# Kernel optimization log

Measured on AMD Instinct MI355X. Metric: run time of the kernel, lower is better.

The kernel has to match this reference:

```python
import jax, jax.numpy as jnp
import numpy as np

D_MODEL = 1024
N_HEADS = 16
HEAD_DIM = D_MODEL // N_HEADS


def setup_inputs() -> dict:
    key = jax.random.key(0)
    ks = jax.random.split(key, 6)
    B, S = 2, 2048
    scale = 1.0 / np.sqrt(D_MODEL)
    x = jax.random.normal(ks[0], (B, S, D_MODEL), dtype=jnp.float32)
    Wq = jax.random.normal(ks[1], (D_MODEL, D_MODEL), dtype=jnp.float32) * scale
    Wk = jax.random.normal(ks[2], (D_MODEL, D_MODEL), dtype=jnp.float32) * scale
    Wv = jax.random.normal(ks[3], (D_MODEL, D_MODEL), dtype=jnp.float32) * scale
    Wo = jax.random.normal(ks[4], (D_MODEL, D_MODEL), dtype=jnp.float32) * scale
    bo = jax.random.normal(ks[5], (D_MODEL,), dtype=jnp.float32) * 0.02
    return {"x": x, "Wq": Wq, "Wk": Wk, "Wv": Wv, "Wo": Wo, "bo": bo}


def reference(x, Wq, Wk, Wv, Wo, bo):
    B, S, _ = x.shape
    H, hd = N_HEADS, HEAD_DIM
    # qkv projections (no bias, qkv_bias=False)
    q = (x @ Wq).reshape(B, S, H, hd).transpose(0, 2, 1, 3)  # [B,H,S,hd]
    k = (x @ Wk).reshape(B, S, H, hd).transpose(0, 2, 1, 3)
    v = (x @ Wv).reshape(B, S, H, hd).transpose(0, 2, 1, 3)
    scores = jnp.einsum('bhqd,bhkd->bhqk', q, k)  # [B,H,S,S]
    causal = jnp.tril(jnp.ones((S, S), dtype=bool))  # True = keep
    scores = jnp.where(causal, scores, -jnp.inf)
    weights = jax.nn.softmax(scores / np.sqrt(hd), axis=-1)
    # dropout p=0.0 -> identity
    ctx = jnp.einsum('bhqk,bhkd->bhqd', weights, v)  # [B,H,S,hd]
    ctx = ctx.transpose(0, 2, 1, 3).reshape(B, S, H * hd)
    return ctx @ Wo + bo
```

## Files before the change

### kernel.cpp

```cpp
#include <hip/hip_runtime.h>
#include <hip/hip_bf16.h>
#include <stdint.h>

#define SEQ    2048
#define BATCH  2
#define DMODEL 1024
#define NHEADS 16
#define HDIM   64
#define MROWS  (BATCH*SEQ)

typedef __attribute__((ext_vector_type(8))) short bf16x8;
typedef __attribute__((ext_vector_type(4))) short bf16x4;
typedef __attribute__((ext_vector_type(4))) float f32x4;

__device__ inline void global_to_lds16(const void* g, void* l) {
  __builtin_amdgcn_global_load_lds(
      (const __attribute__((address_space(1))) uint32_t*)g,
      (__attribute__((address_space(3))) uint32_t*)l, 16, 0, 0);
}

__device__ inline unsigned short f2bf_bits(float f) {
  __hip_bfloat16 h = __float2bfloat16(f);
  return *(unsigned short*)&h;
}

__global__ void prep_kernel(const float* __restrict__ x, __hip_bfloat16* __restrict__ xb,
                            const float* __restrict__ Wq, const float* __restrict__ Wk,
                            const float* __restrict__ Wv, const float* __restrict__ Wo,
                            __hip_bfloat16* __restrict__ Wqkv_t, __hip_bfloat16* __restrict__ Wo_t) {
  __shared__ float tile[32][33];
  if (blockIdx.x < 4096) {
    int i = (blockIdx.x * 256 + threadIdx.x) * 4;
    float4 v = *(const float4*)(x + i);
    ushort4 o;
    o.x = f2bf_bits(v.x); o.y = f2bf_bits(v.y);
    o.z = f2bf_bits(v.z); o.w = f2bf_bits(v.w);
    *(ushort4*)(xb + i) = o;
    return;
  }
  int idx = blockIdx.x - 4096;
  int z = idx >> 10;
  int rem = idx & 1023;
  const float* W = (z == 0) ? Wq : (z == 1) ? Wk : (z == 2) ? Wv : Wo;
  __hip_bfloat16* dst = (z < 3) ? (Wqkv_t + (size_t)z * 1024 * 1024) : Wo_t;
  int k0 = (rem & 31) * 32, n0 = (rem >> 5) * 32;
  int tx = threadIdx.x & 31, ty = threadIdx.x >> 5;
#pragma unroll
  for (int r = 0; r < 4; r++)
    tile[ty + r * 8][tx] = W[(size_t)(k0 + ty + r * 8) * 1024 + n0 + tx];
  __syncthreads();
#pragma unroll
  for (int r = 0; r < 4; r++)
    dst[(size_t)(n0 + ty + r * 8) * 1024 + k0 + tx] = __float2bfloat16(tile[tx][ty + r * 8]);
}

template <int TN, bool OUT_BF16, int MINW, bool FUSE_VT>
__global__ __launch_bounds__(256, MINW)
void gemm_kernel(const __hip_bfloat16* __restrict__ A, const __hip_bfloat16* __restrict__ Bt,
                 void* __restrict__ C, const float* __restrict__ bias, int ldc,
                 __hip_bfloat16* __restrict__ Vt) {
  __shared__ __hip_bfloat16 Asl[2][128 * 64];
  __shared__ __hip_bfloat16 Bsl[2][TN * 64];

  const int t = threadIdx.x;
  const int lane = t & 63;
  const int w = t >> 6;
  constexpr int MI = (TN == 128) ? 4 : 2;
  const int wrow = (TN == 128) ? (w >> 1) * 64 : w * 32;
  const int wcol = (TN == 128) ? (w & 1) * 64 : 0;
  const int m0 = blockIdx.y * 128;
  const int n0 = blockIdx.x * TN;

  f32x4 acc[MI][4];
#pragma unroll
  for (int i = 0; i < MI; i++)
#pragma unroll
    for (int j = 0; j < 4; j++) acc[i][j] = (f32x4){0.f, 0.f, 0.f, 0.f};

  const int srow = lane >> 3;
  const int sjc = (lane & 7) ^ srow;
  const int fm = lane & 15;
  const int g4 = lane >> 4;

  auto stage = [&](int k0, int bufi) {
#pragma unroll
    for (int i = 0; i < 4; i++) {
      int seg = i * 4 + w;
      int r = seg * 8 + srow;
      global_to_lds16(A + (size_t)(m0 + r) * 1024 + k0 + sjc * 8,
                      (void*)(&Asl[bufi][0] + seg * 512 + lane * 8));
    }
#pragma unroll
    for (int i = 0; i < TN / 32; i++) {
      int seg = i * 4 + w;
      int r = seg * 8 + srow;
      global_to_lds16(Bt + (size_t)(n0 + r) * 1024 + k0 + sjc * 8,
                      (void*)(&Bsl[bufi][0] + seg * 512 + lane * 8));
    }
  };

  stage(0, 0);
  for (int k0 = 0; k0 < 1024; k0 += 64) {
    const int buf = (k0 >> 6) & 1;
    __syncthreads();

    bf16x8 af[2][MI], bfr[2][4];
#pragma unroll
    for (int kb = 0; kb < 2; kb++) {
#pragma unroll
      for (int mi = 0; mi < MI; mi++) {
        int row = wrow + mi * 16 + fm;
        af[kb][mi] = *(const bf16x8*)(&Asl[buf][0] + row * 64 + (((kb * 4 + g4) ^ (row & 7)) << 3));
      }
#pragma unroll
      for (int ni = 0; ni < 4; ni++) {
        int row = wcol + ni * 16 + fm;
        bfr[kb][ni] = *(const bf16x8*)(&Bsl[buf][0] + row * 64 + (((kb * 4 + g4) ^ (row & 7)) << 3));
      }
    }

    if (k0 + 64 < 1024) stage(k0 + 64, buf ^ 1);

#pragma unroll
    for (int kb = 0; kb < 2; kb++)
#pragma unroll
      for (int mi = 0; mi < MI; mi++)
#pragma unroll
        for (int ni = 0; ni < 4; ni++)
          acc[mi][ni] = __builtin_amdgcn_mfma_f32_16x16x32_bf16(af[kb][mi], bfr[kb][ni], acc[mi][ni], 0, 0, 0);
  }

  const bool vt_block = FUSE_VT && (n0 >= 2048);
#pragma unroll
  for (int mi = 0; mi < MI; mi++) {
    int mb = m0 + wrow + mi * 16 + g4 * 4;
#pragma unroll
    for (int ni = 0; ni < 4; ni++) {
      int n = n0 + wcol + ni * 16 + fm;
      if (vt_block) {
        int nv = n - 2048;
        int bhh = (mb >> 11) * 16 + (nv >> 6);
        int d = nv & 63;
        int s = mb & 2047;
        unsigned short u[4];
#pragma unroll
        for (int r = 0; r < 4; r++) u[r] = f2bf_bits(acc[mi][ni][r]);
        *(ushort4*)(Vt + ((size_t)bhh * 64 + d) * 2048 + s) = *(const ushort4*)u;
      } else {
        float bv = OUT_BF16 ? 0.f : bias[n];
#pragma unroll
        for (int r = 0; r < 4; r++) {
          if (OUT_BF16)
            ((__hip_bfloat16*)C)[(size_t)(mb + r) * ldc + n] = __float2bfloat16(acc[mi][ni][r]);
          else
            ((float*)C)[(size_t)(mb + r) * ldc + n] = acc[mi][ni][r] + bv;
        }
      }
    }
  }
}

__global__ __launch_bounds__(512, 2)
void qkv_gemm_kernel(const __hip_bfloat16* __restrict__ A,
                     const __hip_bfloat16* __restrict__ Bt,
                     __hip_bfloat16* __restrict__ QKV,
                     __hip_bfloat16* __restrict__ Vt) {
  extern __shared__ __align__(128) char smem_raw[];
  __hip_bfloat16* Asl = (__hip_bfloat16*)smem_raw;
  __hip_bfloat16* Bsl = Asl + 4 * 8192;

  const int t = threadIdx.x;
  const int lane = t & 63;
  const int w = t >> 6;
  const int wm = w >> 2;
  const int wn = w & 3;

  const int wgid = blockIdx.y * 12 + blockIdx.x;
  const int swz = (wgid & 7) * 24 + (wgid >> 3);
  const int m0 = (swz / 12) * 256;
  const int n0 = (swz % 12) * 256;

  const int fm = lane & 15;
  const int g4 = lane >> 4;
  const int rsl = ((g4 ^ ((fm >> 1) & 3)) << 3);
  const int rr = lane >> 2;
  const int cc = (lane & 3) ^ ((lane >> 3) & 3);

  f32x4 acc[8][4];
#pragma unroll
  for (int i = 0; i < 8; i++)
#pragma unroll
    for (int j = 0; j < 4; j++) acc[i][j] = (f32x4){0.f, 0.f, 0.f, 0.f};

  auto stageA = [&](int ktt, int s) {
#pragma unroll
    for (int i = 0; i < 2; i++) {
      int seg = w * 2 + i;
      global_to_lds16(A + (size_t)(m0 + seg * 16 + rr) * 1024 + ktt * 32 + cc * 8,
                      (void*)(Asl + s * 8192 + seg * 512 + lane * 8));
    }
  };
  auto stageB = [&](int ktt, int s) {
#pragma unroll
    for (int i = 0; i < 2; i++) {
      int seg = w * 2 + i;
      global_to_lds16(Bt + (size_t)(n0 + seg * 16 + rr) * 1024 + ktt * 32 + cc * 8,
                      (void*)(Bsl + s * 8192 + seg * 512 + lane * 8));
    }
  };

  stageA(0, 0); stageB(0, 0);
  stageA(1, 1); stageB(1, 1);
  stageA(2, 2); stageB(2, 2);
  asm volatile("s_waitcnt vmcnt(8)" ::: "memory");
  __builtin_amdgcn_s_barrier();

  for (int kt = 0; kt < 32; ++kt) {
    const int s = kt & 3;
    const __hip_bfloat16* Ab = Asl + s * 8192;
    const __hip_bfloat16* Bb = Bsl + s * 8192;

    bf16x8 af[4], bf[4];
#pragma unroll
    for (int mi = 0; mi < 4; mi++) {
      int row = wm * 128 + mi * 16 + fm;
      af[mi] = *(const bf16x8*)(Ab + row * 32 + rsl);
    }
#pragma unroll
    for (int ni = 0; ni < 4; ni++) {
      int row = wn * 64 + ni * 16 + fm;
      bf[ni] = *(const bf16x8*)(Bb + row * 32 + rsl);
    }
    if (kt < 29) stageA(kt + 3, (kt + 3) & 3);
    __builtin_amdgcn_s_barrier();
    __builtin_amdgcn_s_setprio(1);
#pragma unroll
    for (int mi = 0; mi < 4; mi++)
#pragma unroll
      for (int ni = 0; ni < 4; ni++)
        acc[mi][ni] = __builtin_amdgcn_mfma_f32_16x16x32_bf16(af[mi], bf[ni], acc[mi][ni], 0, 0, 0);
    __builtin_amdgcn_s_setprio(0);
    __builtin_amdgcn_s_barrier();

#pragma unroll
    for (int mi = 0; mi < 4; mi++) {
      int row = wm * 128 + (mi + 4) * 16 + fm;
      af[mi] = *(const bf16x8*)(Ab + row * 32 + rsl);
    }
    if (kt < 29) stageB(kt + 3, (kt + 3) & 3);
    __builtin_amdgcn_s_barrier();
    __builtin_amdgcn_s_setprio(1);
#pragma unroll
    for (int mi = 0; mi < 4; mi++)
#pragma unroll
      for (int ni = 0; ni < 4; ni++)
        acc[mi + 4][ni] = __builtin_amdgcn_mfma_f32_16x16x32_bf16(af[mi], bf[ni], acc[mi + 4][ni], 0, 0, 0);
    __builtin_amdgcn_s_setprio(0);
    if (kt < 29)       asm volatile("s_waitcnt vmcnt(8)" ::: "memory");
    else if (kt == 29) asm volatile("s_waitcnt vmcnt(4)" ::: "memory");
    else if (kt == 30) asm volatile("s_waitcnt vmcnt(0)" ::: "memory");
    __builtin_amdgcn_s_barrier();
  }

  const bool vt_block = (n0 >= 2048);
#pragma unroll
  for (int mi = 0; mi < 8; mi++) {
    int mb = m0 + wm * 128 + mi * 16 + g4 * 4;
#pragma unroll
    for (int ni = 0; ni < 4; ni++) {
      int n = n0 + wn * 64 + ni * 16 + fm;
      if (vt_block) {
        int nv = n - 2048;
        int bhh = (mb >> 11) * 16 + (nv >> 6);
        int d = nv & 63;
        int ssq = mb & 2047;
        unsigned short u[4];
#pragma unroll
        for (int r = 0; r < 4; r++) u[r] = f2bf_bits(acc[mi][ni][r]);
        *(ushort4*)(Vt + ((size_t)bhh * 64 + d) * 2048 + ssq) = *(const ushort4*)u;
      } else {
#pragma unroll
        for (int r = 0; r < 4; r++)
          QKV[(size_t)(mb + r) * 3072 + n] = __float2bfloat16(acc[mi][ni][r]);
      }
    }
  }
}

__global__ __launch_bounds__(256, 2)
void attn_kernel(const __hip_bfloat16* __restrict__ QKV,
                 const __hip_bfloat16* __restrict__ Vt,
                 __hip_bfloat16* __restrict__ ctx) {
  __shared__ __hip_bfloat16 Klds[2][128 * 64];
  __shared__ __hip_bfloat16 Vlds[2][64 * 128];

  const int t = threadIdx.x;
  const int lane = t & 63;
  const int w = t >> 6;
  const int L = blockIdx.x;
  const int bh = (L & 7) + 8 * ((L >> 3) & 3);
  const int jraw = L >> 5;
  const int jb = (jraw < 8) ? jraw : 23 - jraw;
  const int qtab[2] = { jb, 31 - jb };
  const int b = bh >> 4, h = bh & 15;
  const int fm = lane & 15;
  const int g4 = lane >> 4;
  const int fk = g4 * 8;
  const size_t rowb = (size_t)b * SEQ;
  const float c = 0.18033688011112042f;

  const int krr = lane >> 3;
  const int kjc = (lane & 7) ^ krr;
  const int vrr = lane >> 4;

  bf16x8 qf[2][2];
#pragma unroll
  for (int hh = 0; hh < 2; hh++) {
    const __hip_bfloat16* qp = QKV + (rowb + qtab[hh] * 64 + w * 16 + fm) * 3072 + h * 64 + fk;
    bf16x8 r0 = *(const bf16x8*)qp;
    bf16x8 r1 = *(const bf16x8*)(qp + 32);
#pragma unroll
    for (int i = 0; i < 8; i++) {
      float f0 = __uint_as_float(((unsigned)(unsigned short)r0[i]) << 16) * c;
      float f1 = __uint_as_float(((unsigned)(unsigned short)r1[i]) << 16) * c;
      r0[i] = (short)f2bf_bits(f0);
      r1[i] = (short)f2bf_bits(f1);
    }
    qf[hh][0] = r0; qf[hh][1] = r1;
  }

  bf16x4 ones4;
#pragma unroll
  for (int i = 0; i < 4; i++) ones4[i] = (short)0x3F80;

  f32x4 acc[2][4];
  f32x4 lacc[2];
#pragma unroll
  for (int hh = 0; hh < 2; hh++) {
    lacc[hh] = (f32x4){0.f, 0.f, 0.f, 0.f};
#pragma unroll
    for (int d = 0; d < 4; d++) acc[hh][d] = (f32x4){0.f, 0.f, 0.f, 0.f};
  }

  auto stage = [&](int pt, int bufi) {
    const int kt0 = pt * 128;
#pragma unroll
    for (int i = 0; i < 4; i++) {
      int seg = i * 4 + w;
      int kr = seg * 8 + krr;
      global_to_lds16(QKV + (rowb + kt0 + kr) * 3072 + 1024 + h * 64 + kjc * 8,
                      (void*)(&Klds[bufi][0] + seg * 512 + lane * 8));
      int vd = seg * 4 + vrr;
      int vjc = (lane & 15) ^ ((seg & 1) * 4 + vrr);
      global_to_lds16(Vt + ((size_t)bh * 64 + vd) * 2048 + kt0 + vjc * 8,
                      (void*)(&Vlds[bufi][0] + seg * 512 + lane * 8));
    }
  };

  auto subcompute = [&](const bf16x8 (&kf)[2][4], const bf16x4 (&vf)[4][4], int kts) {
    const bool act0 = (kts <= qtab[0]);
    f32x4 st1[4], st0[4];
#pragma unroll
    for (int ns = 0; ns < 4; ns++) {
      st1[ns] = (f32x4){0.f, 0.f, 0.f, 0.f};
      st0[ns] = (f32x4){0.f, 0.f, 0.f, 0.f};
    }
#pragma unroll
    for (int kk = 0; kk < 2; kk++) {
#pragma unroll
      for (int ns = 0; ns < 4; ns++)
        st1[ns] = __builtin_amdgcn_mfma_f32_16x16x32_bf16(kf[kk][ns], qf[1][kk], st1[ns], 0, 0, 0);
      if (act0)
#pragma unroll
        for (int ns = 0; ns < 4; ns++)
          st0[ns] = __builtin_amdgcn_mfma_f32_16x16x32_bf16(kf[kk][ns], qf[0][kk], st0[ns], 0, 0, 0);
    }
    auto half = [&](const f32x4 (&st)[4], int hh) {
      const bool diag = (kts == qtab[hh]);
#pragma unroll
      for (int ns = 0; ns < 4; ns++) {
        float e[4];
#pragma unroll
        for (int r = 0; r < 4; r++) {
          float p = __builtin_amdgcn_exp2f(st[ns][r]);
          if (diag) {
            int ktl = ns * 16 + g4 * 4 + r;
            p = (ktl > w * 16 + fm) ? 0.f : p;
          }
          e[r] = p;
        }
        unsigned lo = __builtin_amdgcn_perm(__builtin_bit_cast(unsigned, e[1]),
                                            __builtin_bit_cast(unsigned, e[0]), 0x07060302u);
        unsigned hi = __builtin_amdgcn_perm(__builtin_bit_cast(unsigned, e[3]),
                                            __builtin_bit_cast(unsigned, e[2]), 0x07060302u);
        uint2 pp; pp.x = lo; pp.y = hi;
        bf16x4 pf = __builtin_bit_cast(bf16x4, pp);
        lacc[hh] = __builtin_amdgcn_mfma_f32_16x16x16bf16_1k(pf, ones4, lacc[hh], 0, 0, 0);
#pragma unroll
        for (int dd = 0; dd < 4; dd++)
          acc[hh][dd] = __builtin_amdgcn_mfma_f32_16x16x16bf16_1k(pf, vf[dd][ns], acc[hh][dd], 0, 0, 0);
      }
    };
    half(st1, 1);
    if (act0) half(st0, 0);
  };

  auto load_kf = [&](const __hip_bfloat16* Kb, int sc, bf16x8 (&kf)[2][4]) {
#pragma unroll
    for (int kk = 0; kk < 2; kk++)
#pragma unroll
      for (int ns = 0; ns < 4; ns++) {
        int row = sc * 64 + ns * 16 + fm;
        kf[kk][ns] = *(const bf16x8*)(Kb + row * 64 + (((kk * 4 + g4) ^ (fm & 7)) << 3));
      }
  };
  auto load_vf = [&](const __hip_bfloat16* Vb, int sc, bf16x4 (&vf)[4][4]) {
#pragma unroll
    for (int dd = 0; dd < 4; dd++)
#pragma unroll
      for (int ns = 0; ns < 4; ns++) {
        int ch = sc * 8 + ns * 2 + (g4 >> 1);
        vf[dd][ns] = *(const bf16x4*)(Vb + (dd * 16 + fm) * 128 +
                                      ((ch ^ (fm & 7)) << 3) + (g4 & 1) * 4);
      }
  };

  const int lastt = qtab[1];
  const int lastp = lastt >> 1;
  stage(0, 0);
  for (int pt = 0; pt <= lastp; ++pt) {
    __syncthreads();
    const int buf = pt & 1;
    const __hip_bfloat16* Kb = &Klds[buf][0];
    const __hip_bfloat16* Vb = &Vlds[buf][0];

    bf16x8 kf[2][4];
    bf16x4 vf[4][4];
    load_kf(Kb, 0, kf);
    load_vf(Vb, 0, vf);
    if (pt < lastp) stage(pt + 1, buf ^ 1);
    subcompute(kf, vf, pt * 2);

    if (pt * 2 + 1 <= lastt) {
      load_kf(Kb, 1, kf);
      load_vf(Vb, 1, vf);
      subcompute(kf, vf, pt * 2 + 1);
    }
  }

#pragma unroll
  for (int hh = 0; hh < 2; hh++) {
    float rl[4];
#pragma unroll
    for (int r = 0; r < 4; r++) rl[r] = __builtin_amdgcn_rcpf(lacc[hh][r]);
#pragma unroll
    for (int dd = 0; dd < 4; dd++)
#pragma unroll
      for (int r = 0; r < 4; r++) {
        int q = qtab[hh] * 64 + w * 16 + g4 * 4 + r;
        ctx[(rowb + q) * 1024 + h * 64 + dd * 16 + fm] =
            __float2bfloat16(acc[hh][dd][r] * rl[r]);
      }
  }
}

extern "C" void kernel_launch(void* const* d_in, const int* in_sizes, int n_in,
                              void* d_out, int out_size, void* d_ws, size_t ws_size,
                              hipStream_t stream) {
  const float* x  = (const float*)d_in[0];
  const float* Wq = (const float*)d_in[1];
  const float* Wk = (const float*)d_in[2];
  const float* Wv = (const float*)d_in[3];
  const float* Wo = (const float*)d_in[4];
  const float* bo = (const float*)d_in[5];
  float* out = (float*)d_out;

  char* ws = (char*)d_ws;
  __hip_bfloat16* xb     = (__hip_bfloat16*)(ws);
  __hip_bfloat16* Wqkv_t = (__hip_bfloat16*)(ws + (8ull  << 20));
  __hip_bfloat16* Wo_t   = (__hip_bfloat16*)(ws + (14ull << 20));
  __hip_bfloat16* QKV    = (__hip_bfloat16*)(ws + (16ull << 20));
  __hip_bfloat16* ctxb   = (__hip_bfloat16*)(ws + (40ull << 20));
  __hip_bfloat16* Vt     = (__hip_bfloat16*)(ws + (48ull << 20));

  static int qkv_attr_done = 0;
  if (!qkv_attr_done) {
    (void)hipFuncSetAttribute((const void*)qkv_gemm_kernel,
                              hipFuncAttributeMaxDynamicSharedMemorySize, 131072);
    qkv_attr_done = 1;
  }

  prep_kernel<<<dim3(8192), dim3(256), 0, stream>>>(x, xb, Wq, Wk, Wv, Wo, Wqkv_t, Wo_t);
  qkv_gemm_kernel<<<dim3(12, 16), dim3(512), 131072, stream>>>(xb, Wqkv_t, QKV, Vt);
  attn_kernel<<<dim3(512), dim3(256), 0, stream>>>(QKV, Vt, ctxb);
  gemm_kernel<64, false, 2, false><<<dim3(16, 32), dim3(256), 0, stream>>>(
      ctxb, Wo_t, (void*)out, bo, 1024, nullptr);
}
```

Measured before the change: 171.2 us.

## Switch QKV GEMM to BK=64 double-buffered pipeline with 8-way XOR swizzle

Changes the QKV projection GEMM from a 4-stage, K=32 ring buffer to a 2-stage, K=64 double buffer. Each tile row now spans 64 bf16 values with an 8-way XOR swizzle on the 16-byte column chunks, and each K-tile runs four MFMA phases. The aim is to halve the loop trip count and the barriers per unit of K while keeping LDS size the same. The trade-off is a shallower prefetch: only one tile is in flight and there is a full vmcnt(0) wait every iteration, which may expose global-load latency.

```diff
diff --git a/kernel.cpp b/kernel.cpp
--- a/kernel.cpp
+++ b/kernel.cpp
@@ -167,7 +167,7 @@
                      __hip_bfloat16* __restrict__ Vt) {
   extern __shared__ __align__(128) char smem_raw[];
   __hip_bfloat16* Asl = (__hip_bfloat16*)smem_raw;
-  __hip_bfloat16* Bsl = Asl + 4 * 8192;
+  __hip_bfloat16* Bsl = Asl + 2 * 16384;
 
   const int t = threadIdx.x;
   const int lane = t & 63;
@@ -182,9 +182,7 @@
 
   const int fm = lane & 15;
   const int g4 = lane >> 4;
-  const int rsl = ((g4 ^ ((fm >> 1) & 3)) << 3);
-  const int rr = lane >> 2;
-  const int cc = (lane & 3) ^ ((lane >> 3) & 3);
+  const int csrc = (lane & 7) ^ ((lane >> 3) & 7);
 
   f32x4 acc[8][4];
 #pragma unroll
@@ -192,46 +190,53 @@
 #pragma unroll
     for (int j = 0; j < 4; j++) acc[i][j] = (f32x4){0.f, 0.f, 0.f, 0.f};
 
-  auto stageA = [&](int ktt, int s) {
-#pragma unroll
-    for (int i = 0; i < 2; i++) {
-      int seg = w * 2 + i;
-      global_to_lds16(A + (size_t)(m0 + seg * 16 + rr) * 1024 + ktt * 32 + cc * 8,
-                      (void*)(Asl + s * 8192 + seg * 512 + lane * 8));
-    }
-  };
-  auto stageB = [&](int ktt, int s) {
-#pragma unroll
-    for (int i = 0; i < 2; i++) {
-      int seg = w * 2 + i;
-      global_to_lds16(Bt + (size_t)(n0 + seg * 16 + rr) * 1024 + ktt * 32 + cc * 8,
-                      (void*)(Bsl + s * 8192 + seg * 512 + lane * 8));
-    }
-  };
-
-  stageA(0, 0); stageB(0, 0);
-  stageA(1, 1); stageB(1, 1);
-  stageA(2, 2); stageB(2, 2);
-  asm volatile("s_waitcnt vmcnt(8)" ::: "memory");
-  __builtin_amdgcn_s_barrier();
-
-  for (int kt = 0; kt < 32; ++kt) {
-    const int s = kt & 3;
-    const __hip_bfloat16* Ab = Asl + s * 8192;
-    const __hip_bfloat16* Bb = Bsl + s * 8192;
-
-    bf16x8 af[4], bf[4];
+  auto stageA = [&](int ktt, int bufi) {
+#pragma unroll
+    for (int j = 0; j < 4; j++) {
+      int seg = w * 4 + j;
+      int row = seg * 8 + (lane >> 3);
+      global_to_lds16(A + (size_t)(m0 + row) * 1024 + ktt * 64 + csrc * 8,
+                      (void*)(Asl + bufi * 16384 + seg * 512 + lane * 8));
+    }
+  };
+  auto stageB = [&](int ktt, int bufi) {
+#pragma unroll
+    for (int j = 0; j < 4; j++) {
+      int seg = w * 4 + j;
+      int row = seg * 8 + (lane >> 3);
+      global_to_lds16(Bt + (size_t)(n0 + row) * 1024 + ktt * 64 + csrc * 8,
+                      (void*)(Bsl + bufi * 16384 + seg * 512 + lane * 8));
+    }
+  };
+
+  auto load_af = [&](const __hip_bfloat16* Ab, int mi0, int kk, bf16x8 (&af)[4]) {
 #pragma unroll
     for (int mi = 0; mi < 4; mi++) {
-      int row = wm * 128 + mi * 16 + fm;
-      af[mi] = *(const bf16x8*)(Ab + row * 32 + rsl);
-    }
+      int row = wm * 128 + (mi0 + mi) * 16 + fm;
+      af[mi] = *(const bf16x8*)(Ab + row * 64 + (((kk * 4 + g4) ^ (fm & 7)) << 3));
+    }
+  };
+  auto load_bf = [&](const __hip_bfloat16* Bb, int kk, bf16x8 (&bf)[4]) {
 #pragma unroll
     for (int ni = 0; ni < 4; ni++) {
       int row = wn * 64 + ni * 16 + fm;
-      bf[ni] = *(const bf16x8*)(Bb + row * 32 + rsl);
-    }
-    if (kt < 29) stageA(kt + 3, (kt + 3) & 3);
+      bf[ni] = *(const bf16x8*)(Bb + row * 64 + (((kk * 4 + g4) ^ (fm & 7)) << 3));
+    }
+  };
+
+  stageA(0, 0); stageB(0, 0);
+  asm volatile("s_waitcnt vmcnt(0)" ::: "memory");
+  __builtin_amdgcn_s_barrier();
+
+  for (int kt = 0; kt < 16; ++kt) {
+    const int buf = kt & 1;
+    const __hip_bfloat16* Ab = Asl + buf * 16384;
+    const __hip_bfloat16* Bb = Bsl + buf * 16384;
+    bf16x8 af[4], bf[4];
+
+    load_af(Ab, 0, 0, af);
+    load_bf(Bb, 0, bf);
+    if (kt < 15) stageA(kt + 1, buf ^ 1);
     __builtin_amdgcn_s_barrier();
     __builtin_amdgcn_s_setprio(1);
 #pragma unroll
@@ -242,12 +247,8 @@
     __builtin_amdgcn_s_setprio(0);
     __builtin_amdgcn_s_barrier();
 
-#pragma unroll
-    for (int mi = 0; mi < 4; mi++) {
-      int row = wm * 128 + (mi + 4) * 16 + fm;
-      af[mi] = *(const bf16x8*)(Ab + row * 32 + rsl);
-    }
-    if (kt < 29) stageB(kt + 3, (kt + 3) & 3);
+    load_af(Ab, 4, 0, af);
+    if (kt < 15) stageB(kt + 1, buf ^ 1);
     __builtin_amdgcn_s_barrier();
     __builtin_amdgcn_s_setprio(1);
 #pragma unroll
@@ -256,9 +257,30 @@
       for (int ni = 0; ni < 4; ni++)
         acc[mi + 4][ni] = __builtin_amdgcn_mfma_f32_16x16x32_bf16(af[mi], bf[ni], acc[mi + 4][ni], 0, 0, 0);
     __builtin_amdgcn_s_setprio(0);
-    if (kt < 29)       asm volatile("s_waitcnt vmcnt(8)" ::: "memory");
-    else if (kt == 29) asm volatile("s_waitcnt vmcnt(4)" ::: "memory");
-    else if (kt == 30) asm volatile("s_waitcnt vmcnt(0)" ::: "memory");
+    __builtin_amdgcn_s_barrier();
+
+    load_af(Ab, 0, 1, af);
+    load_bf(Bb, 1, bf);
+    __builtin_amdgcn_s_barrier();
+    __builtin_amdgcn_s_setprio(1);
+#pragma unroll
+    for (int mi = 0; mi < 4; mi++)
+#pragma unroll
+      for (int ni = 0; ni < 4; ni++)
+        acc[mi][ni] = __builtin_amdgcn_mfma_f32_16x16x32_bf16(af[mi], bf[ni], acc[mi][ni], 0, 0, 0);
+    __builtin_amdgcn_s_setprio(0);
+    __builtin_amdgcn_s_barrier();
+
+    load_af(Ab, 4, 1, af);
+    __builtin_amdgcn_s_barrier();
+    __builtin_amdgcn_s_setprio(1);
+#pragma unroll
+    for (int mi = 0; mi < 4; mi++)
+#pragma unroll
+      for (int ni = 0; ni < 4; ni++)
+        acc[mi + 4][ni] = __builtin_amdgcn_mfma_f32_16x16x32_bf16(af[mi], bf[ni], acc[mi + 4][ni], 0, 0, 0);
+    __builtin_amdgcn_s_setprio(0);
+    asm volatile("s_waitcnt vmcnt(0)" ::: "memory");
     __builtin_amdgcn_s_barrier();
   }
 
```

New measurement: 168.5 us. Within noise of the previous version (-1.5%).

## Restructure QKV GEMM into BK=64 double-buffered half-tile pipeline with 8-way swizzle

Applied to the files above, without the earlier changes.

Rewrites the QKV projection GEMM to use a K-tile of 64 instead of 32. The 256x256 block tile is split into 128-row A and B halves, each staged separately into a two-deep LDS ring with an XOR swizzle over 8 chunks. The main loop interleaves eight 16-MFMA quadrant phases with per-half global-to-LDS prefetches, which halves the number of K iterations and spreads load issue across compute phases. In exchange there are more barriers per K step, a different warp-to-tile mapping, and a hand-tuned vmcnt wait schedule that must match the issue order to stay correct.

```diff
diff --git a/kernel.cpp b/kernel.cpp
--- a/kernel.cpp
+++ b/kernel.cpp
@@ -54,6 +54,175 @@
     dst[(size_t)(n0 + ty + r * 8) * 1024 + k0 + tx] = __float2bfloat16(tile[tx][ty + r * 8]);
 }
 
+__global__ __launch_bounds__(512, 2)
+void qkv_gemm_kernel(const __hip_bfloat16* __restrict__ A,
+                     const __hip_bfloat16* __restrict__ Bt,
+                     __hip_bfloat16* __restrict__ QKV,
+                     __hip_bfloat16* __restrict__ Vt) {
+  extern __shared__ __align__(128) char smem_raw[];
+  __hip_bfloat16* lds = (__hip_bfloat16*)smem_raw;
+
+  const int t = threadIdx.x;
+  const int lane = t & 63;
+  const int w = t >> 6;
+  const int wm = w >> 2;
+  const int wn = w & 3;
+
+  const int wgid = blockIdx.y * 12 + blockIdx.x;
+  const int swz = (wgid & 7) * 24 + (wgid >> 3);
+  const int m0 = (swz / 12) * 256;
+  const int n0 = (swz % 12) * 256;
+
+  const int fm = lane & 15;
+  const int g4 = lane >> 4;
+  const int csrc = (lane & 7) ^ ((lane >> 3) & 7);
+
+  f32x4 acc[8][4];
+#pragma unroll
+  for (int i = 0; i < 8; i++)
+#pragma unroll
+    for (int j = 0; j < 4; j++) acc[i][j] = (f32x4){0.f, 0.f, 0.f, 0.f};
+
+  auto stage_half = [&](int op, int half, int kt) {
+    const __hip_bfloat16* src = op ? Bt : A;
+    const int base = op ? n0 : m0;
+    const int slot = ((kt & 1) * 4 + op * 2 + half) * 8192;
+#pragma unroll
+    for (int j = 0; j < 2; j++) {
+      int seg = w * 2 + j;
+      int rh = seg * 8 + (lane >> 3);
+      global_to_lds16(src + (size_t)(base + half * 128 + rh) * 1024 + kt * 64 + csrc * 8,
+                      (void*)(lds + slot + seg * 512 + lane * 8));
+    }
+  };
+
+  auto load_af = [&](int dbuf, int mh, bf16x8 (&af)[2][4]) {
+    const int slot = (dbuf * 4 + mh) * 8192;
+#pragma unroll
+    for (int kk = 0; kk < 2; kk++)
+#pragma unroll
+      for (int mi = 0; mi < 4; mi++) {
+        int rh = wm * 64 + mi * 16 + fm;
+        af[kk][mi] = *(const bf16x8*)(lds + slot + rh * 64 + (((kk * 4 + g4) ^ (fm & 7)) << 3));
+      }
+  };
+  auto load_bf = [&](int dbuf, int nh, bf16x8 (&bf)[2][2]) {
+    const int slot = (dbuf * 4 + 2 + nh) * 8192;
+#pragma unroll
+    for (int kk = 0; kk < 2; kk++)
+#pragma unroll
+      for (int ni = 0; ni < 2; ni++) {
+        int rh = wn * 32 + ni * 16 + fm;
+        bf[kk][ni] = *(const bf16x8*)(lds + slot + rh * 64 + (((kk * 4 + g4) ^ (fm & 7)) << 3));
+      }
+  };
+
+  auto mfma16 = [&](int mh, int nh, const bf16x8 (&af)[2][4], const bf16x8 (&bf)[2][2]) {
+    __builtin_amdgcn_s_setprio(1);
+#pragma unroll
+    for (int kk = 0; kk < 2; kk++)
+#pragma unroll
+      for (int mi = 0; mi < 4; mi++)
+#pragma unroll
+        for (int ni = 0; ni < 2; ni++)
+          acc[mh * 4 + mi][nh * 2 + ni] = __builtin_amdgcn_mfma_f32_16x16x32_bf16(
+              af[kk][mi], bf[kk][ni], acc[mh * 4 + mi][nh * 2 + ni], 0, 0, 0);
+    __builtin_amdgcn_s_setprio(0);
+  };
+
+  stage_half(0, 0, 0); stage_half(1, 0, 0); stage_half(1, 1, 0); stage_half(0, 1, 0);
+  stage_half(0, 0, 1); stage_half(1, 1, 1);
+  asm volatile("s_waitcnt vmcnt(4)" ::: "memory");
+  __builtin_amdgcn_s_barrier();
+
+  for (int kt = 0; kt < 16; kt += 2) {
+    const bool pf = (kt < 14);
+    bf16x8 af[2][4], bf[2][2], bf2[2][2];
+
+    load_af(0, 0, af);
+    load_bf(0, 0, bf);
+    stage_half(1, 0, kt + 1);
+    __builtin_amdgcn_s_barrier();
+    mfma16(0, 0, af, bf);
+    __builtin_amdgcn_s_barrier();
+
+    load_bf(0, 1, bf2);
+    stage_half(0, 1, kt + 1);
+    __builtin_amdgcn_s_barrier();
+    mfma16(0, 1, af, bf2);
+    __builtin_amdgcn_s_barrier();
+
+    load_af(0, 1, af);
+    if (pf) stage_half(0, 0, kt + 2);
+    __builtin_amdgcn_s_barrier();
+    mfma16(1, 1, af, bf2);
+    __builtin_amdgcn_s_barrier();
+
+    load_bf(0, 0, bf);
+    if (pf) stage_half(1, 1, kt + 2);
+    __builtin_amdgcn_s_barrier();
+    mfma16(1, 0, af, bf);
+    if (pf) asm volatile("s_waitcnt vmcnt(4)" ::: "memory");
+    else    asm volatile("s_waitcnt vmcnt(0)" ::: "memory");
+    __builtin_amdgcn_s_barrier();
+
+    load_af(1, 0, af);
+    load_bf(1, 0, bf);
+    if (pf) stage_half(1, 0, kt + 2);
+    __builtin_amdgcn_s_barrier();
+    mfma16(0, 0, af, bf);
+    __builtin_amdgcn_s_barrier();
+
+    load_bf(1, 1, bf2);
+    if (pf) stage_half(0, 1, kt + 2);
+    __builtin_amdgcn_s_barrier();
+    mfma16(0, 1, af, bf2);
+    __builtin_amdgcn_s_barrier();
+
+    load_af(1, 1, af);
+    if (pf) stage_half(0, 0, kt + 3);
+    __builtin_amdgcn_s_barrier();
+    mfma16(1, 1, af, bf2);
+    __builtin_amdgcn_s_barrier();
+
+    load_bf(1, 0, bf);
+    if (pf) stage_half(1, 1, kt + 3);
+    __builtin_amdgcn_s_barrier();
+    mfma16(1, 0, af, bf);
+    if (pf) asm volatile("s_waitcnt vmcnt(4)" ::: "memory");
+    __builtin_amdgcn_s_barrier();
+  }
+
+  const bool vt_block = (n0 >= 2048);
+#pragma unroll
+  for (int mh = 0; mh < 2; mh++)
+#pragma unroll
+    for (int mi = 0; mi < 4; mi++) {
+      int mb = m0 + mh * 128 + wm * 64 + mi * 16 + g4 * 4;
+#pragma unroll
+      for (int nh = 0; nh < 2; nh++)
+#pragma unroll
+        for (int ni = 0; ni < 2; ni++) {
+          int n = n0 + nh * 128 + wn * 32 + ni * 16 + fm;
+          f32x4 a = acc[mh * 4 + mi][nh * 2 + ni];
+          if (vt_block) {
+            int nv = n - 2048;
+            int bhh = (mb >> 11) * 16 + (nv >> 6);
+            int d = nv & 63;
+            int ssq = mb & 2047;
+            unsigned short u[4];
+#pragma unroll
+            for (int r = 0; r < 4; r++) u[r] = f2bf_bits(a[r]);
+            *(ushort4*)(Vt + ((size_t)bhh * 64 + d) * 2048 + ssq) = *(const ushort4*)u;
+          } else {
+#pragma unroll
+            for (int r = 0; r < 4; r++)
+              QKV[(size_t)(mb + r) * 3072 + n] = __float2bfloat16(a[r]);
+          }
+        }
+    }
+}
+
 template <int TN, bool OUT_BF16, int MINW, bool FUSE_VT>
 __global__ __launch_bounds__(256, MINW)
 void gemm_kernel(const __hip_bfloat16* __restrict__ A, const __hip_bfloat16* __restrict__ Bt,
@@ -155,133 +324,6 @@
           else
             ((float*)C)[(size_t)(mb + r) * ldc + n] = acc[mi][ni][r] + bv;
         }
-      }
-    }
-  }
-}
-
-__global__ __launch_bounds__(512, 2)
-void qkv_gemm_kernel(const __hip_bfloat16* __restrict__ A,
-                     const __hip_bfloat16* __restrict__ Bt,
-                     __hip_bfloat16* __restrict__ QKV,
-                     __hip_bfloat16* __restrict__ Vt) {
-  extern __shared__ __align__(128) char smem_raw[];
-  __hip_bfloat16* Asl = (__hip_bfloat16*)smem_raw;
-  __hip_bfloat16* Bsl = Asl + 4 * 8192;
-
-  const int t = threadIdx.x;
-  const int lane = t & 63;
-  const int w = t >> 6;
-  const int wm = w >> 2;
-  const int wn = w & 3;
-
-  const int wgid = blockIdx.y * 12 + blockIdx.x;
-  const int swz = (wgid & 7) * 24 + (wgid >> 3);
-  const int m0 = (swz / 12) * 256;
-  const int n0 = (swz % 12) * 256;
-
-  const int fm = lane & 15;
-  const int g4 = lane >> 4;
-  const int rsl = ((g4 ^ ((fm >> 1) & 3)) << 3);
-  const int rr = lane >> 2;
-  const int cc = (lane & 3) ^ ((lane >> 3) & 3);
-
-  f32x4 acc[8][4];
-#pragma unroll
-  for (int i = 0; i < 8; i++)
-#pragma unroll
-    for (int j = 0; j < 4; j++) acc[i][j] = (f32x4){0.f, 0.f, 0.f, 0.f};
-
-  auto stageA = [&](int ktt, int s) {
-#pragma unroll
-    for (int i = 0; i < 2; i++) {
-      int seg = w * 2 + i;
-      global_to_lds16(A + (size_t)(m0 + seg * 16 + rr) * 1024 + ktt * 32 + cc * 8,
-                      (void*)(Asl + s * 8192 + seg * 512 + lane * 8));
-    }
-  };
-  auto stageB = [&](int ktt, int s) {
-#pragma unroll
-    for (int i = 0; i < 2; i++) {
-      int seg = w * 2 + i;
-      global_to_lds16(Bt + (size_t)(n0 + seg * 16 + rr) * 1024 + ktt * 32 + cc * 8,
-                      (void*)(Bsl + s * 8192 + seg * 512 + lane * 8));
-    }
-  };
-
-  stageA(0, 0); stageB(0, 0);
-  stageA(1, 1); stageB(1, 1);
-  stageA(2, 2); stageB(2, 2);
-  asm volatile("s_waitcnt vmcnt(8)" ::: "memory");
-  __builtin_amdgcn_s_barrier();
-
-  for (int kt = 0; kt < 32; ++kt) {
-    const int s = kt & 3;
-    const __hip_bfloat16* Ab = Asl + s * 8192;
-    const __hip_bfloat16* Bb = Bsl + s * 8192;
-
-    bf16x8 af[4], bf[4];
-#pragma unroll
-    for (int mi = 0; mi < 4; mi++) {
-      int row = wm * 128 + mi * 16 + fm;
-      af[mi] = *(const bf16x8*)(Ab + row * 32 + rsl);
-    }
-#pragma unroll
-    for (int ni = 0; ni < 4; ni++) {
-      int row = wn * 64 + ni * 16 + fm;
-      bf[ni] = *(const bf16x8*)(Bb + row * 32 + rsl);
-    }
-    if (kt < 29) stageA(kt + 3, (kt + 3) & 3);
-    __builtin_amdgcn_s_barrier();
-    __builtin_amdgcn_s_setprio(1);
-#pragma unroll
-    for (int mi = 0; mi < 4; mi++)
-#pragma unroll
-      for (int ni = 0; ni < 4; ni++)
-        acc[mi][ni] = __builtin_amdgcn_mfma_f32_16x16x32_bf16(af[mi], bf[ni], acc[mi][ni], 0, 0, 0);
-    __builtin_amdgcn_s_setprio(0);
-    __builtin_amdgcn_s_barrier();
-
-#pragma unroll
-    for (int mi = 0; mi < 4; mi++) {
-      int row = wm * 128 + (mi + 4) * 16 + fm;
-      af[mi] = *(const bf16x8*)(Ab + row * 32 + rsl);
-    }
-    if (kt < 29) stageB(kt + 3, (kt + 3) & 3);
-    __builtin_amdgcn_s_barrier();
-    __builtin_amdgcn_s_setprio(1);
-#pragma unroll
-    for (int mi = 0; mi < 4; mi++)
-#pragma unroll
-      for (int ni = 0; ni < 4; ni++)
-        acc[mi + 4][ni] = __builtin_amdgcn_mfma_f32_16x16x32_bf16(af[mi], bf[ni], acc[mi + 4][ni], 0, 0, 0);
-    __builtin_amdgcn_s_setprio(0);
-    if (kt < 29)       asm volatile("s_waitcnt vmcnt(8)" ::: "memory");
-    else if (kt == 29) asm volatile("s_waitcnt vmcnt(4)" ::: "memory");
-    else if (kt == 30) asm volatile("s_waitcnt vmcnt(0)" ::: "memory");
-    __builtin_amdgcn_s_barrier();
-  }
-
-  const bool vt_block = (n0 >= 2048);
-#pragma unroll
-  for (int mi = 0; mi < 8; mi++) {
-    int mb = m0 + wm * 128 + mi * 16 + g4 * 4;
-#pragma unroll
-    for (int ni = 0; ni < 4; ni++) {
-      int n = n0 + wn * 64 + ni * 16 + fm;
-      if (vt_block) {
-        int nv = n - 2048;
-        int bhh = (mb >> 11) * 16 + (nv >> 6);
-        int d = nv & 63;
-        int ssq = mb & 2047;
-        unsigned short u[4];
-#pragma unroll
-        for (int r = 0; r < 4; r++) u[r] = f2bf_bits(acc[mi][ni][r]);
-        *(ushort4*)(Vt + ((size_t)bhh * 64 + d) * 2048 + ssq) = *(const ushort4*)u;
-      } else {
-#pragma unroll
-        for (int r = 0; r < 4; r++)
-          QKV[(size_t)(mb + r) * 3072 + n] = __float2bfloat16(acc[mi][ni][r]);
       }
     }
   }
```

Result: no change. 170.9 us (-0.1%).
